# Optimization experiments

Measured on AMD Instinct MI355X. Metric: run time of the kernel, lower is better.

## Reference

```python
import jax, jax.numpy as jnp
import numpy as np

DIM = 768
H = 12          # num_heads
KV = 4          # kv_heads
D = DIM // H    # head_dim = 64
ROPE_BASE = 10000.0
WINDOW = 8
B, N = 4, 1024


def setup_inputs() -> dict:
    key = jax.random.key(0)
    ks = jax.random.split(key, 8)
    s = 0.02  # weight scale for sane magnitudes
    return {
        "x": jax.random.normal(ks[0], (B, N, DIM), jnp.float32),
        "Wq": jax.random.normal(ks[1], (2 * DIM, DIM), jnp.float32) * s,
        "Wk": jax.random.normal(ks[2], (2 * DIM * KV // H, DIM), jnp.float32) * s,
        "Wv1": jax.random.normal(ks[3], (DIM * KV // H, DIM), jnp.float32) * s,
        "Wv2": jax.random.normal(ks[4], (DIM * KV // H, DIM), jnp.float32) * s,
        "lambda_p": jnp.full((H, 1, 1), -2.0, jnp.float32),
        "Wo": jax.random.normal(ks[5], (DIM, DIM), jnp.float32) * s,
        "bo": jax.random.normal(ks[6], (DIM,), jnp.float32) * s,
    }


def _rotate_half(x):
    x1 = x[..., ::2]
    x2 = x[..., 1::2]
    return jnp.stack([-x2, x1], axis=-1).reshape(x.shape)


def _rope_cos_sin(n, dtype):
    side = int(n ** 0.5)
    if side * side == n:
        h = np.arange(side, dtype=np.float32)
        gh, gw = np.meshgrid(h, h, indexing="ij")
        pos_h, pos_w = gh.reshape(-1), gw.reshape(-1)
    else:
        pos_h = np.arange(n, dtype=np.float32)
        pos_w = np.zeros_like(pos_h)
    dim_half = D // 2
    inv_freq = ROPE_BASE ** (-np.arange(dim_half, dtype=np.float32) / dim_half)
    theta = np.concatenate([pos_h[:, None] * inv_freq[None, :],
                            pos_w[:, None] * inv_freq[None, :]], axis=1)  # [N, D]
    cos = jnp.asarray(np.cos(theta), dtype)[None, None]  # [1,1,N,D]
    sin = jnp.asarray(np.sin(theta), dtype)[None, None]
    return cos, sin


def _apply_rope(q, cos, sin):
    return q * cos + _rotate_half(q) * sin


def _qk_norm(t):
    return t / (jnp.linalg.norm(t, axis=-1, keepdims=True) + 1e-6)


def _window_mask(n, dtype):
    side = int(n ** 0.5)
    if side * side == n:
        h = np.arange(side)
        gh, gw = np.meshgrid(h, h, indexing="ij")
        coords = np.stack([gh.reshape(-1), gw.reshape(-1)], axis=1)  # [N,2]
        dist = np.abs(coords[:, None, :] - coords[None, :, :]).max(-1)  # Chebyshev
    else:
        idx = np.arange(n)
        dist = np.abs(idx[None, :] - idx[:, None])
    return jnp.asarray(np.where(dist > WINDOW, -np.inf, 0.0).astype(np.float32), dtype)


def _attend(q, k, v, mask):
    # q,k,v: [B,H,N,D]; mask additive [N,N]
    scale = 1.0 / np.sqrt(D)
    scores = jnp.einsum("bhnd,bhmd->bhnm", q, k) * scale + mask
    return jnp.einsum("bhnm,bhmd->bhnd", jax.nn.softmax(scores, axis=-1), v)


def reference(x, Wq, Wk, Wv1, Wv2, lambda_p, Wo, bo):
    b, n, c = x.shape
    rep = H // KV
    q = (x @ Wq.T).reshape(b, n, 2, H, D).transpose(2, 0, 3, 1, 4)   # [2,B,H,N,D]
    k = (x @ Wk.T).reshape(b, n, 2, KV, D).transpose(2, 0, 3, 1, 4)  # [2,B,KV,N,D]
    v1 = (x @ Wv1.T).reshape(b, n, KV, D).transpose(0, 2, 1, 3)      # [B,KV,N,D]
    v2 = (x @ Wv2.T).reshape(b, n, KV, D).transpose(0, 2, 1, 3)
    q1, q2 = q[0], q[1]
    k1, k2 = k[0], k[1]
    # GQA: repeat_interleave over head axis
    k1 = jnp.repeat(k1, rep, axis=1)
    k2 = jnp.repeat(k2, rep, axis=1)
    v1 = jnp.repeat(v1, rep, axis=1)
    v2 = jnp.repeat(v2, rep, axis=1)
    cos, sin = _rope_cos_sin(n, x.dtype)
    q1, q2 = _apply_rope(q1, cos, sin), _apply_rope(q2, cos, sin)
    k1, k2 = _apply_rope(k1, cos, sin), _apply_rope(k2, cos, sin)
    q1, q2, k1, k2 = _qk_norm(q1), _qk_norm(q2), _qk_norm(k1), _qk_norm(k2)
    mask = _window_mask(n, x.dtype)
    out1 = _attend(q1, k1, v1, mask)
    out2 = _attend(q2, k2, v2, mask)
    lam = jax.nn.softplus(lambda_p)  # [H,1,1] broadcasts over [B,H,N,D]
    out = out1 - lam[None] * out2
    out = out.transpose(0, 2, 1, 3).reshape(b, n, c)
    return out @ Wo.T + bo
```

## Files before the change

kernel.cpp:

```cpp
#include <hip/hip_runtime.h>
#include <hip/hip_bf16.h>

#define BATCH 4
#define NSEQ  1024
#define DIM   768
#define NH    12
#define NKV   4
#define HD    64
#define NTOK  (BATCH*NSEQ)

using bf16 = __hip_bfloat16;
typedef __attribute__((ext_vector_type(8))) short short8;
typedef __attribute__((ext_vector_type(4))) float floatx4;
typedef __attribute__((ext_vector_type(4))) unsigned uint4v;

__device__ __forceinline__ float b2f(short x) {
  unsigned u = ((unsigned)(unsigned short)x) << 16;
  return __builtin_bit_cast(float, u);
}
__device__ __forceinline__ unsigned short f2b(float f) {
  unsigned u = __builtin_bit_cast(unsigned, f);
  unsigned r = u + 0x7FFF + ((u >> 16) & 1);
  return (unsigned short)(r >> 16);
}
__device__ __forceinline__ unsigned cvtpk(float lo, float hi) {
  unsigned r;
  asm("v_cvt_pk_bf16_f32 %0, %1, %2" : "=v"(r) : "v"(lo), "v"(hi));
  return r;
}

__device__ __forceinline__ void load_lds_16(const bf16* g, bf16* l) {
  __builtin_amdgcn_global_load_lds(
      (const __attribute__((address_space(1))) void*)g,
      (__attribute__((address_space(3))) void*)l, 16, 0, 0);
}

__global__ __launch_bounds__(256) void cvt_all(
    const float* __restrict__ x,  const float* __restrict__ wq,
    const float* __restrict__ wk, const float* __restrict__ wv1,
    const float* __restrict__ wv2, const float* __restrict__ wo,
    bf16* __restrict__ xb,  bf16* __restrict__ wqb, bf16* __restrict__ wkb,
    bf16* __restrict__ wv1b, bf16* __restrict__ wv2b, bf16* __restrict__ wob)
{
  int i = blockIdx.x * 256 + threadIdx.x;
  const float* s; bf16* d; int off;
  if      (i <  786432) { s = x;   d = xb;   off = i; }
  else if (i < 1081344) { s = wq;  d = wqb;  off = i -  786432; }
  else if (i < 1179648) { s = wk;  d = wkb;  off = i - 1081344; }
  else if (i < 1228800) { s = wv1; d = wv1b; off = i - 1179648; }
  else if (i < 1277952) { s = wv2; d = wv2b; off = i - 1228800; }
  else                  { s = wo;  d = wob;  off = i - 1277952; }
  float4 f = reinterpret_cast<const float4*>(s)[off];
  ushort4 u;
  u.x = f2b(f.x); u.y = f2b(f.y); u.z = f2b(f.z); u.w = f2b(f.w);
  reinterpret_cast<ushort4*>(d)[off] = u;
}

__global__ __launch_bounds__(256, 3) void gemm_qkv(
    const bf16* __restrict__ xb,
    const bf16* __restrict__ Wqb, const bf16* __restrict__ Wkb,
    const bf16* __restrict__ Wv1b, const bf16* __restrict__ Wv2b,
    bf16* __restrict__ Qpk, bf16* __restrict__ Kpk,
    bf16* __restrict__ Vpk1, bf16* __restrict__ Vpk2)
{
  __shared__ __align__(16) bf16 As[128 * 64];
  __shared__ __align__(16) bf16 Ws[128 * 64];

  const int bn = blockIdx.x, bm = blockIdx.y;
  const bf16* Wp;
  if (bn < 12)      Wp = Wqb  + (size_t)bn * 128 * 768;
  else if (bn < 16) Wp = Wkb  + (size_t)(bn - 12) * 128 * 768;
  else if (bn < 18) Wp = Wv1b + (size_t)(bn - 16) * 128 * 768;
  else              Wp = Wv2b + (size_t)(bn - 18) * 128 * 768;

  const int t = threadIdx.x, wave = t >> 6, lane = t & 63;
  const int wm = wave >> 1, wn = wave & 1;
  const int quad = lane >> 4, lr = lane & 15;

  const int srow = wave * 32 + (lane >> 3);
  const int scol = ((lane & 7) ^ (lane >> 3)) * 8;
  const bf16* Ag = xb + (size_t)(bm * 128 + srow) * 768 + scol;
  const bf16* Wg = Wp + (size_t)srow * 768 + scol;
  bf16* Al = As + wave * 32 * 64;
  bf16* Wl = Ws + wave * 32 * 64;

  floatx4 acc[4][4] = {};

  for (int k0 = 0; k0 < 768; k0 += 64) {
    #pragma unroll
    for (int c = 0; c < 4; ++c) {
      load_lds_16(Ag + (size_t)c * 8 * 768 + k0, Al + c * 8 * 64);
      load_lds_16(Wg + (size_t)c * 8 * 768 + k0, Wl + c * 8 * 64);
    }
    __syncthreads();

    short8 af[4][2], wf[4][2];
    #pragma unroll
    for (int mt = 0; mt < 4; ++mt)
      #pragma unroll
      for (int ks = 0; ks < 2; ++ks)
        af[mt][ks] = *reinterpret_cast<const short8*>(
            &As[(wm * 64 + mt * 16 + lr) * 64 + ((ks * 32 + quad * 8) ^ ((lr & 7) * 8))]);
    #pragma unroll
    for (int nt = 0; nt < 4; ++nt)
      #pragma unroll
      for (int ks = 0; ks < 2; ++ks)
        wf[nt][ks] = *reinterpret_cast<const short8*>(
            &Ws[(wn * 64 + nt * 16 + lr) * 64 + ((ks * 32 + quad * 8) ^ ((lr & 7) * 8))]);

    #pragma unroll
    for (int mt = 0; mt < 4; ++mt)
      #pragma unroll
      for (int nt = 0; nt < 4; ++nt) {
        acc[mt][nt] = __builtin_amdgcn_mfma_f32_16x16x32_bf16(af[mt][0], wf[nt][0], acc[mt][nt], 0, 0, 0);
        acc[mt][nt] = __builtin_amdgcn_mfma_f32_16x16x32_bf16(af[mt][1], wf[nt][1], acc[mt][nt], 0, 0, 0);
      }
    __syncthreads();
  }

  if (bn < 16) {
    const float K2 = 0.41524101186098309f;
    const float invf0 = exp2f(-(float)lr * K2);
    const float invf1 = exp2f(-(float)(16 + lr) * K2);
    const float sgn = (lr & 1) ? 1.f : -1.f;
    const bool isq = (bn < 12);
    const int hq = bn * 2 + wn;
    const int sq_ = hq / 12, hq_ = hq % 12;
    const int hh = (bn - 12) * 2 + wn;
    const int sk_ = hh >> 2, kvh_ = hh & 3;
    const int qk128 = (lr >> 3) * 128;
    #pragma unroll
    for (int mt = 0; mt < 4; ++mt) {
      const int row0 = bm * 128 + wm * 64 + mt * 16 + quad * 4;
      const int n0 = row0 & (NSEQ - 1);
      const int bb = row0 >> 10, kh = n0 >> 5;
      const float ph = (float)kh;
      const float pw0 = (float)(n0 & 31);
      const float t0 = ph * invf0, t1 = ph * invf1;
      const float c0 = __cosf(t0), s0 = __sinf(t0);
      const float c1 = __cosf(t1), s1 = __sinf(t1);
      bf16* tb0;
      if (isq) {
        tb0 = Qpk + ((size_t)((bb * 2 + sq_) * 12 + hq_) * 32 + kh) * 2048
              + (size_t)(mt & 1) * 1024 + qk128 + (quad * 4) * 8 + (lr & 7);
      } else {
        tb0 = Kpk + ((size_t)((bb * 2 + sk_) * 4 + kvh_) * 32 + kh) * 2048
              + (size_t)(mt & 1) * 1024 + qk128 + (quad * 4) * 8 + (lr & 7);
      }
      #pragma unroll
      for (int r = 0; r < 4; ++r) {
        float v0 = acc[mt][0][r];
        float v1 = acc[mt][1][r];
        float v2 = acc[mt][2][r];
        float v3 = acc[mt][3][r];
        float rot0 = sgn * __shfl_xor(v0, 1);
        float rot1 = sgn * __shfl_xor(v1, 1);
        float rot2 = sgn * __shfl_xor(v2, 1);
        float rot3 = sgn * __shfl_xor(v3, 1);
        float pw = pw0 + (float)r;
        float t2 = pw * invf0, t3 = pw * invf1;
        float rv0 = v0 * c0 + rot0 * s0;
        float rv1 = v1 * c1 + rot1 * s1;
        float rv2 = v2 * __cosf(t2) + rot2 * __sinf(t2);
        float rv3 = v3 * __cosf(t3) + rot3 * __sinf(t3);
        float ss = rv0 * rv0 + rv1 * rv1 + rv2 * rv2 + rv3 * rv3;
        #pragma unroll
        for (int off = 1; off < 16; off <<= 1) ss += __shfl_xor(ss, off);
        float sc = 1.f / (sqrtf(ss) + 1e-6f);
        if (isq) sc *= 0.18033688011112042f;
        bf16* tb = tb0 + r * 8;
        unsigned pkA = cvtpk(rv0 * sc, rv1 * sc);
        unsigned pkB = cvtpk(rv2 * sc, rv3 * sc);
        *(unsigned short*)&tb[0]   = (unsigned short)pkA;
        *(unsigned short*)&tb[256] = (unsigned short)(pkA >> 16);
        *(unsigned short*)&tb[512] = (unsigned short)pkB;
        *(unsigned short*)&tb[768] = (unsigned short)(pkB >> 16);
      }
    }
  } else {
    const bool is2 = (bn >= 18);
    bf16* Vp = is2 ? Vpk2 : Vpk1;
    const int kvh_ = (bn - (is2 ? 18 : 16)) * 2 + wn;
    #pragma unroll
    for (int mt = 0; mt < 4; ++mt)
      #pragma unroll
      for (int r = 0; r < 4; ++r) {
        int row = bm * 128 + wm * 64 + mt * 16 + quad * 4 + r;
        int n = row & (NSEQ - 1);
        int bb = row >> 10, kh = n >> 5;
        int rowm = (mt & 1) * 16 + quad * 4 + r;
        int quad_v = (rowm >> 2) & 3;
        int j = ((rowm >> 4) << 2) | (rowm & 3);
        bf16* tb = Vp + ((size_t)(bb * 4 + kvh_) * 32 + kh) * 2048
                   + quad_v * 128 + lr * 8 + j;
        unsigned pkA = cvtpk(acc[mt][0][r], acc[mt][1][r]);
        unsigned pkB = cvtpk(acc[mt][2][r], acc[mt][3][r]);
        *(unsigned short*)&tb[0]    = (unsigned short)pkA;
        *(unsigned short*)&tb[512]  = (unsigned short)(pkA >> 16);
        *(unsigned short*)&tb[1024] = (unsigned short)pkB;
        *(unsigned short*)&tb[1536] = (unsigned short)(pkB >> 16);
      }
  }
}

__global__ __launch_bounds__(256) void gemm_out(
    const bf16* __restrict__ Xb, const bf16* __restrict__ Wob,
    float* __restrict__ out, const float* __restrict__ bias)
{
  __shared__ __align__(16) bf16 As[64 * 64];
  __shared__ __align__(16) bf16 Ws[64 * 64];

  const int bn = blockIdx.x, bm = blockIdx.y;
  const int t = threadIdx.x, wave = t >> 6, lane = t & 63;
  const int wm = wave >> 1, wn = wave & 1;
  const int quad = lane >> 4, lr = lane & 15;

  const int srow = wave * 16 + (lane >> 3);
  const int scol = ((lane & 7) ^ (lane >> 3)) * 8;
  const bf16* Ag = Xb  + (size_t)(bm * 64 + srow) * 768 + scol;
  const bf16* Wg = Wob + (size_t)(bn * 64 + srow) * 768 + scol;
  bf16* Al = As + wave * 16 * 64;
  bf16* Wl = Ws + wave * 16 * 64;

  floatx4 acc[2][2] = {};

  for (int k0 = 0; k0 < 768; k0 += 64) {
    #pragma unroll
    for (int c = 0; c < 2; ++c) {
      load_lds_16(Ag + (size_t)c * 8 * 768 + k0, Al + c * 8 * 64);
      load_lds_16(Wg + (size_t)c * 8 * 768 + k0, Wl + c * 8 * 64);
    }
    __syncthreads();

    short8 af[2][2], wf[2][2];
    #pragma unroll
    for (int mt = 0; mt < 2; ++mt)
      #pragma unroll
      for (int ks = 0; ks < 2; ++ks)
        af[mt][ks] = *reinterpret_cast<const short8*>(
            &As[(wm * 32 + mt * 16 + lr) * 64 + ((ks * 32 + quad * 8) ^ ((lr & 7) * 8))]);
    #pragma unroll
    for (int nt = 0; nt < 2; ++nt)
      #pragma unroll
      for (int ks = 0; ks < 2; ++ks)
        wf[nt][ks] = *reinterpret_cast<const short8*>(
            &Ws[(wn * 32 + nt * 16 + lr) * 64 + ((ks * 32 + quad * 8) ^ ((lr & 7) * 8))]);

    #pragma unroll
    for (int mt = 0; mt < 2; ++mt)
      #pragma unroll
      for (int nt = 0; nt < 2; ++nt) {
        acc[mt][nt] = __builtin_amdgcn_mfma_f32_16x16x32_bf16(af[mt][0], wf[nt][0], acc[mt][nt], 0, 0, 0);
        acc[mt][nt] = __builtin_amdgcn_mfma_f32_16x16x32_bf16(af[mt][1], wf[nt][1], acc[mt][nt], 0, 0, 0);
      }
    __syncthreads();
  }

  #pragma unroll
  for (int nt = 0; nt < 2; ++nt) {
    int col = bn * 64 + wn * 32 + nt * 16 + lr;
    float bv = bias[col];
    #pragma unroll
    for (int mt = 0; mt < 2; ++mt)
      #pragma unroll
      for (int r = 0; r < 4; ++r) {
        int row = bm * 64 + wm * 32 + mt * 16 + quad * 4 + r;
        out[(size_t)row * 768 + col] = acc[mt][nt][r] + bv;
      }
  }
}

struct Frag { short8 kf[2][2]; short8 vf[4]; };

__device__ __forceinline__ void attn_load(
    Frag& f, const bf16* __restrict__ kp, const bf16* __restrict__ vp,
    int kh, int lane8)
{
  const bf16* kt = kp + (size_t)kh * 2048 + lane8;
  const bf16* vt = vp + (size_t)kh * 2048 + lane8;
  f.kf[0][0] = *reinterpret_cast<const short8*>(kt);
  f.kf[0][1] = *reinterpret_cast<const short8*>(kt + 512);
  f.kf[1][0] = *reinterpret_cast<const short8*>(kt + 1024);
  f.kf[1][1] = *reinterpret_cast<const short8*>(kt + 1536);
  f.vf[0] = *reinterpret_cast<const short8*>(vt);
  f.vf[1] = *reinterpret_cast<const short8*>(vt + 512);
  f.vf[2] = *reinterpret_cast<const short8*>(vt + 1024);
  f.vf[3] = *reinterpret_cast<const short8*>(vt + 1536);
}

__device__ __forceinline__ void attn_step(
    const short8 (&qf)[2][2], const Frag& f, const floatx4 (&Sinit)[2][2],
    floatx4 (&O)[2][4], float (&psum)[2])
{
  floatx4 St[2][2] = {{Sinit[0][0], Sinit[0][1]}, {Sinit[1][0], Sinit[1][1]}};
  __builtin_amdgcn_s_setprio(1);
  #pragma unroll
  for (int ks = 0; ks < 2; ++ks) {
    St[0][0] = __builtin_amdgcn_mfma_f32_16x16x32_bf16(f.kf[0][ks], qf[0][ks], St[0][0], 0, 0, 0);
    St[0][1] = __builtin_amdgcn_mfma_f32_16x16x32_bf16(f.kf[0][ks], qf[1][ks], St[0][1], 0, 0, 0);
    St[1][0] = __builtin_amdgcn_mfma_f32_16x16x32_bf16(f.kf[1][ks], qf[0][ks], St[1][0], 0, 0, 0);
    St[1][1] = __builtin_amdgcn_mfma_f32_16x16x32_bf16(f.kf[1][ks], qf[1][ks], St[1][1], 0, 0, 0);
  }
  __builtin_amdgcn_s_setprio(0);

  unsigned pk[2][2][2];
  #pragma unroll
  for (int kt = 0; kt < 2; ++kt)
    #pragma unroll
    for (int mt = 0; mt < 2; ++mt) {
      float pr[4];
      #pragma unroll
      for (int r = 0; r < 4; ++r) {
        float p = __builtin_amdgcn_exp2f(St[kt][mt][r]);
        psum[mt] += p;
        pr[r] = p;
      }
      pk[kt][mt][0] = cvtpk(pr[0], pr[1]);
      pk[kt][mt][1] = cvtpk(pr[2], pr[3]);
    }

  __builtin_amdgcn_s_setprio(1);
  #pragma unroll
  for (int mt = 0; mt < 2; ++mt) {
    uint4v regs;
    regs[0] = pk[0][mt][0];
    regs[1] = pk[0][mt][1];
    regs[2] = pk[1][mt][0];
    regs[3] = pk[1][mt][1];
    short8 pa = __builtin_bit_cast(short8, regs);
    #pragma unroll
    for (int ntd = 0; ntd < 4; ++ntd)
      O[mt][ntd] = __builtin_amdgcn_mfma_f32_16x16x32_bf16(pa, f.vf[ntd], O[mt][ntd], 0, 0, 0);
  }
  __builtin_amdgcn_s_setprio(0);
}

__global__ __launch_bounds__(256, 3) void attn_mfma(
    const bf16* __restrict__ Qpk, const bf16* __restrict__ Kpk,
    const bf16* __restrict__ Vpk1, const bf16* __restrict__ Vpk2,
    const float* __restrict__ lambda_p, bf16* __restrict__ X)
{
  __shared__ __align__(16) char smem[20480];

  const int bid = blockIdx.x;
  const int qh = bid & 31;
  const int hb = bid >> 5;
  const int h  = hb % 12;
  const int b  = hb / 12;
  const int kvh = h / 3;

  const int t = threadIdx.x;
  const int w = t >> 6;
  const int s = w >> 1;
  const int half = w & 1;
  const int lane = t & 63;
  const int quad = lane >> 4, lr = lane & 15;
  const int lane8 = lane * 8;

  float* myO = (float*)(smem + (s ? 10240 : 0));
  float* myP = (float*)(smem + (s ? 10240 : 0) + 8192);
  bf16* Xs = (bf16*)smem;

  const int tok0 = b * NSEQ + qh * 32;

  short8 qf[2][2];
  {
    const bf16* qt = Qpk + ((size_t)((b * 2 + s) * 12 + h) * 32 + qh) * 2048 + lane8;
    qf[0][0] = *reinterpret_cast<const short8*>(qt);
    qf[0][1] = *reinterpret_cast<const short8*>(qt + 512);
    qf[1][0] = *reinterpret_cast<const short8*>(qt + 1024);
    qf[1][1] = *reinterpret_cast<const short8*>(qt + 1536);
  }

  floatx4 Sinit[2][2];
  #pragma unroll
  for (int kt = 0; kt < 2; ++kt)
    #pragma unroll
    for (int mt = 0; mt < 2; ++mt)
      #pragma unroll
      for (int r = 0; r < 4; ++r) {
        int wk = kt * 16 + quad * 4 + r;
        int wq = mt * 16 + lr;
        int d = wk - wq; if (d < 0) d = -d;
        Sinit[kt][mt][r] = (d <= 8) ? 0.0f : -1e38f;
      }

  floatx4 O[2][4] = {};
  float psum[2] = {};

  const int kh0 = (qh > 8) ? qh - 8 : 0;
  const int kh1 = (qh < 23) ? qh + 8 : 31;
  const int cnt = kh1 - kh0 + 1;
  const int cA = (cnt + 1) >> 1;
  const int khA = half ? kh0 + cA : kh0;
  const int khB = half ? kh1 : kh0 + cA - 1;

  const bf16* kpbase = Kpk + (size_t)((b * 2 + s) * 4 + kvh) * 32 * 2048;
  const bf16* vpbase = (s ? Vpk2 : Vpk1) + (size_t)(b * 4 + kvh) * 32 * 2048;

  Frag fA, fB;
  attn_load(fA, kpbase, vpbase, khA, lane8);
  attn_load(fB, kpbase, vpbase, (khA + 1 <= khB) ? khA + 1 : khB, lane8);

  int i = khA;
  while (true) {
    attn_step(qf, fA, Sinit, O, psum);
    if (i == khB) break;
    ++i;
    attn_load(fA, kpbase, vpbase, (i + 1 <= khB) ? i + 1 : i, lane8);
    attn_step(qf, fB, Sinit, O, psum);
    if (i == khB) break;
    ++i;
    attn_load(fB, kpbase, vpbase, (i + 1 <= khB) ? i + 1 : i, lane8);
  }

  auto writeslab = [&]() {
    #pragma unroll
    for (int mt = 0; mt < 2; ++mt)
      #pragma unroll
      for (int ntd = 0; ntd < 4; ++ntd)
        *reinterpret_cast<floatx4*>(&myO[(mt * 4 + ntd) * 256 + lane * 4]) = O[mt][ntd];
    myP[lane]      = psum[0];
    myP[64 + lane] = psum[1];
  };
  auto readadd_norm = [&]() {
    #pragma unroll
    for (int mt = 0; mt < 2; ++mt)
      #pragma unroll
      for (int ntd = 0; ntd < 4; ++ntd)
        O[mt][ntd] += *reinterpret_cast<const floatx4*>(&myO[(mt * 4 + ntd) * 256 + lane * 4]);
    psum[0] += myP[lane];
    psum[1] += myP[64 + lane];
    #pragma unroll
    for (int mt = 0; mt < 2; ++mt) {
      psum[mt] += __shfl_xor(psum[mt], 16);
      psum[mt] += __shfl_xor(psum[mt], 32);
      psum[mt] = 1.f / psum[mt];
    }
    #pragma unroll
    for (int mt = 0; mt < 2; ++mt) {
      float invq[4];
      #pragma unroll
      for (int r = 0; r < 4; ++r)
        invq[r] = __shfl(psum[mt], (lane & 48) + quad * 4 + r);
      #pragma unroll
      for (int ntd = 0; ntd < 4; ++ntd)
        #pragma unroll
        for (int r = 0; r < 4; ++r)
          O[mt][ntd][r] *= invq[r];
    }
  };

  __syncthreads();
  if (half) writeslab();
  __syncthreads();
  if (!half) {
    readadd_norm();
    if (s) {
      #pragma unroll
      for (int mt = 0; mt < 2; ++mt)
        #pragma unroll
        for (int ntd = 0; ntd < 4; ++ntd)
          *reinterpret_cast<floatx4*>(&myO[(mt * 4 + ntd) * 256 + lane * 4]) = O[mt][ntd];
    }
  }
  __syncthreads();
  if (w == 0) {
    const float* O2s = (const float*)(smem + 10240);
    float lam = log1pf(__expf(lambda_p[h]));
    #pragma unroll
    for (int mt = 0; mt < 2; ++mt)
      #pragma unroll
      for (int ntd = 0; ntd < 4; ++ntd) {
        floatx4 o2 = *reinterpret_cast<const floatx4*>(&O2s[(mt * 4 + ntd) * 256 + lane * 4]);
        #pragma unroll
        for (int r = 0; r < 4; ++r) {
          float xv = O[mt][ntd][r] - lam * o2[r];
          *(unsigned short*)&Xs[(mt * 16 + quad * 4 + r) * 72 + ntd * 16 + lr] = f2b(xv);
        }
      }
  }
  __syncthreads();

  {
    int row = t >> 3, seg = t & 7;
    short8 xv = *reinterpret_cast<const short8*>(&Xs[row * 72 + seg * 8]);
    *reinterpret_cast<short8*>(X + (size_t)(tok0 + row) * 768 + h * 64 + seg * 8) = xv;
  }
}

extern "C" void kernel_launch(void* const* d_in, const int* in_sizes, int n_in,
                              void* d_out, int out_size, void* d_ws, size_t ws_size,
                              hipStream_t stream)
{
  const float* x        = (const float*)d_in[0];
  const float* Wq       = (const float*)d_in[1];
  const float* Wk       = (const float*)d_in[2];
  const float* Wv1      = (const float*)d_in[3];
  const float* Wv2      = (const float*)d_in[4];
  const float* lambda_p = (const float*)d_in[5];
  const float* Wo       = (const float*)d_in[6];
  const float* bo       = (const float*)d_in[7];
  float* out = (float*)d_out;

  bf16* xb   = (bf16*)d_ws;
  bf16* Wqb  = xb   + (size_t)NTOK * 768;
  bf16* Wkb  = Wqb  + (size_t)1536 * 768;
  bf16* Wv1b = Wkb  + (size_t)512 * 768;
  bf16* Wv2b = Wv1b + (size_t)256 * 768;
  bf16* Wob  = Wv2b + (size_t)256 * 768;
  bf16* Qpk  = Wob  + (size_t)768 * 768;
  bf16* Xb   = Qpk  + (size_t)NTOK * 1536;
  bf16* Vpk1 = Xb   + (size_t)NTOK * 768;
  bf16* Vpk2 = Vpk1 + (size_t)512 * 2048;
  bf16* Kpk  = Vpk2 + (size_t)512 * 2048;

  cvt_all<<<5568, 256, 0, stream>>>(x, Wq, Wk, Wv1, Wv2, Wo,
                                    xb, Wqb, Wkb, Wv1b, Wv2b, Wob);

  gemm_qkv<<<dim3(20, 32), 256, 0, stream>>>(xb, Wqb, Wkb, Wv1b, Wv2b,
                                             Qpk, Kpk, Vpk1, Vpk2);

  attn_mfma<<<BATCH * NH * 32, 256, 0, stream>>>(Qpk, Kpk, Vpk1, Vpk2, lambda_p, Xb);

  gemm_out<<<dim3(12, 64), 256, 0, stream>>>(Xb, Wob, out, bo);
}
```

Measured before the change: 140.8 us.

## Switch windowed attention to 32x32x16 MFMA tiles with repacked Q/K/V layouts

Replaces the 16x16x32 bf16 MFMA tiling in the attention inner loop with 32x32x16 MFMAs, so each wave computes the 32x32 score block with 4 instructions instead of 8 and the PV product with 4 larger ones instead of 8. The QKV projection epilogue is changed to write the packed Q/K/V fragments in the layout the new MFMA operands expect. The softmax row-sum reduction, normalization and output write-back are remapped to the 32x32 accumulator layout. This reduces instruction issue and shuffle overhead, at the cost of larger accumulators (more registers) and longer-latency MFMAs.

```diff
diff --git a/kernel.cpp b/kernel.cpp
--- a/kernel.cpp
+++ b/kernel.cpp
@@ -12,6 +12,7 @@
 using bf16 = __hip_bfloat16;
 typedef __attribute__((ext_vector_type(8))) short short8;
 typedef __attribute__((ext_vector_type(4))) float floatx4;
+typedef __attribute__((ext_vector_type(16))) float floatx16;
 typedef __attribute__((ext_vector_type(4))) unsigned uint4v;
 
 __device__ __forceinline__ float b2f(short x) {
@@ -128,7 +129,7 @@
     const int sq_ = hq / 12, hq_ = hq % 12;
     const int hh = (bn - 12) * 2 + wn;
     const int sk_ = hh >> 2, kvh_ = hh & 3;
-    const int qk128 = (lr >> 3) * 128;
+    const int fo_lr = (lr >> 3) * 256 + (lr & 7);
     #pragma unroll
     for (int mt = 0; mt < 4; ++mt) {
       const int row0 = bm * 128 + wm * 64 + mt * 16 + quad * 4;
@@ -142,10 +143,10 @@
       bf16* tb0;
       if (isq) {
         tb0 = Qpk + ((size_t)((bb * 2 + sq_) * 12 + hq_) * 32 + kh) * 2048
-              + (size_t)(mt & 1) * 1024 + qk128 + (quad * 4) * 8 + (lr & 7);
+              + fo_lr + ((mt & 1) * 16 + quad * 4) * 8;
       } else {
         tb0 = Kpk + ((size_t)((bb * 2 + sk_) * 4 + kvh_) * 32 + kh) * 2048
-              + (size_t)(mt & 1) * 1024 + qk128 + (quad * 4) * 8 + (lr & 7);
+              + fo_lr + ((mt & 1) * 16 + quad * 4) * 8;
       }
       #pragma unroll
       for (int r = 0; r < 4; ++r) {
@@ -171,10 +172,10 @@
         bf16* tb = tb0 + r * 8;
         unsigned pkA = cvtpk(rv0 * sc, rv1 * sc);
         unsigned pkB = cvtpk(rv2 * sc, rv3 * sc);
-        *(unsigned short*)&tb[0]   = (unsigned short)pkA;
-        *(unsigned short*)&tb[256] = (unsigned short)(pkA >> 16);
-        *(unsigned short*)&tb[512] = (unsigned short)pkB;
-        *(unsigned short*)&tb[768] = (unsigned short)(pkB >> 16);
+        *(unsigned short*)&tb[0]    = (unsigned short)pkA;
+        *(unsigned short*)&tb[512]  = (unsigned short)(pkA >> 16);
+        *(unsigned short*)&tb[1024] = (unsigned short)pkB;
+        *(unsigned short*)&tb[1536] = (unsigned short)(pkB >> 16);
       }
     }
   } else {
@@ -189,16 +190,17 @@
         int n = row & (NSEQ - 1);
         int bb = row >> 10, kh = n >> 5;
         int rowm = (mt & 1) * 16 + quad * 4 + r;
-        int quad_v = (rowm >> 2) & 3;
-        int j = ((rowm >> 4) << 2) | (rowm & 3);
+        int s_ = rowm >> 4;
+        int g_ = (rowm >> 2) & 1;
+        int j  = ((rowm >> 3) & 1) * 4 + (rowm & 3);
         bf16* tb = Vp + ((size_t)(bb * 4 + kvh_) * 32 + kh) * 2048
-                   + quad_v * 128 + lr * 8 + j;
+                   + s_ * 512 + (g_ * 32 + lr) * 8 + j;
         unsigned pkA = cvtpk(acc[mt][0][r], acc[mt][1][r]);
         unsigned pkB = cvtpk(acc[mt][2][r], acc[mt][3][r]);
         *(unsigned short*)&tb[0]    = (unsigned short)pkA;
-        *(unsigned short*)&tb[512]  = (unsigned short)(pkA >> 16);
+        *(unsigned short*)&tb[128]  = (unsigned short)(pkA >> 16);
         *(unsigned short*)&tb[1024] = (unsigned short)pkB;
-        *(unsigned short*)&tb[1536] = (unsigned short)(pkB >> 16);
+        *(unsigned short*)&tb[1152] = (unsigned short)(pkB >> 16);
       }
   }
 }
@@ -270,7 +272,7 @@
   }
 }
 
-struct Frag { short8 kf[2][2]; short8 vf[4]; };
+struct Frag { short8 kf[4]; short8 vf[4]; };
 
 __device__ __forceinline__ void attn_load(
     Frag& f, const bf16* __restrict__ kp, const bf16* __restrict__ vp,
@@ -278,10 +280,10 @@
 {
   const bf16* kt = kp + (size_t)kh * 2048 + lane8;
   const bf16* vt = vp + (size_t)kh * 2048 + lane8;
-  f.kf[0][0] = *reinterpret_cast<const short8*>(kt);
-  f.kf[0][1] = *reinterpret_cast<const short8*>(kt + 512);
-  f.kf[1][0] = *reinterpret_cast<const short8*>(kt + 1024);
-  f.kf[1][1] = *reinterpret_cast<const short8*>(kt + 1536);
+  f.kf[0] = *reinterpret_cast<const short8*>(kt);
+  f.kf[1] = *reinterpret_cast<const short8*>(kt + 512);
+  f.kf[2] = *reinterpret_cast<const short8*>(kt + 1024);
+  f.kf[3] = *reinterpret_cast<const short8*>(kt + 1536);
   f.vf[0] = *reinterpret_cast<const short8*>(vt);
   f.vf[1] = *reinterpret_cast<const short8*>(vt + 512);
   f.vf[2] = *reinterpret_cast<const short8*>(vt + 1024);
@@ -289,49 +291,37 @@
 }
 
 __device__ __forceinline__ void attn_step(
-    const short8 (&qf)[2][2], const Frag& f, const floatx4 (&Sinit)[2][2],
-    floatx4 (&O)[2][4], float (&psum)[2])
-{
-  floatx4 St[2][2] = {{Sinit[0][0], Sinit[0][1]}, {Sinit[1][0], Sinit[1][1]}};
+    const short8 (&qf)[4], const Frag& f, const floatx16& Sinit,
+    floatx16 (&O)[2], float& psum)
+{
+  floatx16 St = Sinit;
   __builtin_amdgcn_s_setprio(1);
   #pragma unroll
-  for (int ks = 0; ks < 2; ++ks) {
-    St[0][0] = __builtin_amdgcn_mfma_f32_16x16x32_bf16(f.kf[0][ks], qf[0][ks], St[0][0], 0, 0, 0);
-    St[0][1] = __builtin_amdgcn_mfma_f32_16x16x32_bf16(f.kf[0][ks], qf[1][ks], St[0][1], 0, 0, 0);
-    St[1][0] = __builtin_amdgcn_mfma_f32_16x16x32_bf16(f.kf[1][ks], qf[0][ks], St[1][0], 0, 0, 0);
-    St[1][1] = __builtin_amdgcn_mfma_f32_16x16x32_bf16(f.kf[1][ks], qf[1][ks], St[1][1], 0, 0, 0);
-  }
+  for (int s = 0; s < 4; ++s)
+    St = __builtin_amdgcn_mfma_f32_32x32x16_bf16(f.kf[s], qf[s], St, 0, 0, 0);
   __builtin_amdgcn_s_setprio(0);
 
-  unsigned pk[2][2][2];
+  float p[16];
   #pragma unroll
-  for (int kt = 0; kt < 2; ++kt)
-    #pragma unroll
-    for (int mt = 0; mt < 2; ++mt) {
-      float pr[4];
-      #pragma unroll
-      for (int r = 0; r < 4; ++r) {
-        float p = __builtin_amdgcn_exp2f(St[kt][mt][r]);
-        psum[mt] += p;
-        pr[r] = p;
-      }
-      pk[kt][mt][0] = cvtpk(pr[0], pr[1]);
-      pk[kt][mt][1] = cvtpk(pr[2], pr[3]);
-    }
+  for (int r = 0; r < 16; ++r) {
+    p[r] = __builtin_amdgcn_exp2f(St[r]);
+    psum += p[r];
+  }
+  unsigned pk[8];
+  #pragma unroll
+  for (int i = 0; i < 8; ++i) pk[i] = cvtpk(p[2 * i], p[2 * i + 1]);
+
+  uint4v r0, r1;
+  r0[0] = pk[0]; r0[1] = pk[1]; r0[2] = pk[2]; r0[3] = pk[3];
+  r1[0] = pk[4]; r1[1] = pk[5]; r1[2] = pk[6]; r1[3] = pk[7];
+  short8 pa0 = __builtin_bit_cast(short8, r0);
+  short8 pa1 = __builtin_bit_cast(short8, r1);
 
   __builtin_amdgcn_s_setprio(1);
-  #pragma unroll
-  for (int mt = 0; mt < 2; ++mt) {
-    uint4v regs;
-    regs[0] = pk[0][mt][0];
-    regs[1] = pk[0][mt][1];
-    regs[2] = pk[1][mt][0];
-    regs[3] = pk[1][mt][1];
-    short8 pa = __builtin_bit_cast(short8, regs);
-    #pragma unroll
-    for (int ntd = 0; ntd < 4; ++ntd)
-      O[mt][ntd] = __builtin_amdgcn_mfma_f32_16x16x32_bf16(pa, f.vf[ntd], O[mt][ntd], 0, 0, 0);
-  }
+  O[0] = __builtin_amdgcn_mfma_f32_32x32x16_bf16(pa0, f.vf[0], O[0], 0, 0, 0);
+  O[0] = __builtin_amdgcn_mfma_f32_32x32x16_bf16(pa1, f.vf[1], O[0], 0, 0, 0);
+  O[1] = __builtin_amdgcn_mfma_f32_32x32x16_bf16(pa0, f.vf[2], O[1], 0, 0, 0);
+  O[1] = __builtin_amdgcn_mfma_f32_32x32x16_bf16(pa1, f.vf[3], O[1], 0, 0, 0);
   __builtin_amdgcn_s_setprio(0);
 }
 
@@ -354,7 +344,7 @@
   const int s = w >> 1;
   const int half = w & 1;
   const int lane = t & 63;
-  const int quad = lane >> 4, lr = lane & 15;
+  const int g = lane >> 5, wq = lane & 31;
   const int lane8 = lane * 8;
 
   float* myO = (float*)(smem + (s ? 10240 : 0));
@@ -363,30 +353,25 @@
 
   const int tok0 = b * NSEQ + qh * 32;
 
-  short8 qf[2][2];
+  short8 qf[4];
   {
     const bf16* qt = Qpk + ((size_t)((b * 2 + s) * 12 + h) * 32 + qh) * 2048 + lane8;
-    qf[0][0] = *reinterpret_cast<const short8*>(qt);
-    qf[0][1] = *reinterpret_cast<const short8*>(qt + 512);
-    qf[1][0] = *reinterpret_cast<const short8*>(qt + 1024);
-    qf[1][1] = *reinterpret_cast<const short8*>(qt + 1536);
-  }
-
-  floatx4 Sinit[2][2];
+    qf[0] = *reinterpret_cast<const short8*>(qt);
+    qf[1] = *reinterpret_cast<const short8*>(qt + 512);
+    qf[2] = *reinterpret_cast<const short8*>(qt + 1024);
+    qf[3] = *reinterpret_cast<const short8*>(qt + 1536);
+  }
+
+  floatx16 Sinit;
   #pragma unroll
-  for (int kt = 0; kt < 2; ++kt)
-    #pragma unroll
-    for (int mt = 0; mt < 2; ++mt)
-      #pragma unroll
-      for (int r = 0; r < 4; ++r) {
-        int wk = kt * 16 + quad * 4 + r;
-        int wq = mt * 16 + lr;
-        int d = wk - wq; if (d < 0) d = -d;
-        Sinit[kt][mt][r] = (d <= 8) ? 0.0f : -1e38f;
-      }
-
-  floatx4 O[2][4] = {};
-  float psum[2] = {};
+  for (int reg = 0; reg < 16; ++reg) {
+    int wk = (reg & 3) + 8 * (reg >> 2) + 4 * g;
+    int d = wk - wq; if (d < 0) d = -d;
+    Sinit[reg] = (d <= 8) ? 0.0f : -1e38f;
+  }
+
+  floatx16 O[2] = {};
+  float psum = 0.f;
 
   const int kh0 = (qh > 8) ? qh - 8 : 0;
   const int kh1 = (qh < 23) ? qh + 8 : 31;
@@ -416,39 +401,37 @@
 
   auto writeslab = [&]() {
     #pragma unroll
-    for (int mt = 0; mt < 2; ++mt)
-      #pragma unroll
-      for (int ntd = 0; ntd < 4; ++ntd)
-        *reinterpret_cast<floatx4*>(&myO[(mt * 4 + ntd) * 256 + lane * 4]) = O[mt][ntd];
-    myP[lane]      = psum[0];
-    myP[64 + lane] = psum[1];
+    for (int pv = 0; pv < 2; ++pv)
+      #pragma unroll
+      for (int rq = 0; rq < 4; ++rq) {
+        floatx4 c;
+        c[0] = O[pv][rq * 4 + 0]; c[1] = O[pv][rq * 4 + 1];
+        c[2] = O[pv][rq * 4 + 2]; c[3] = O[pv][rq * 4 + 3];
+        *reinterpret_cast<floatx4*>(&myO[(pv * 4 + rq) * 256 + lane * 4]) = c;
+      }
+    myP[lane] = psum;
   };
   auto readadd_norm = [&]() {
     #pragma unroll
-    for (int mt = 0; mt < 2; ++mt)
-      #pragma unroll
-      for (int ntd = 0; ntd < 4; ++ntd)
-        O[mt][ntd] += *reinterpret_cast<const floatx4*>(&myO[(mt * 4 + ntd) * 256 + lane * 4]);
-    psum[0] += myP[lane];
-    psum[1] += myP[64 + lane];
-    #pragma unroll
-    for (int mt = 0; mt < 2; ++mt) {
-      psum[mt] += __shfl_xor(psum[mt], 16);
-      psum[mt] += __shfl_xor(psum[mt], 32);
-      psum[mt] = 1.f / psum[mt];
-    }
-    #pragma unroll
-    for (int mt = 0; mt < 2; ++mt) {
-      float invq[4];
-      #pragma unroll
-      for (int r = 0; r < 4; ++r)
-        invq[r] = __shfl(psum[mt], (lane & 48) + quad * 4 + r);
-      #pragma unroll
-      for (int ntd = 0; ntd < 4; ++ntd)
-        #pragma unroll
-        for (int r = 0; r < 4; ++r)
-          O[mt][ntd][r] *= invq[r];
-    }
+    for (int pv = 0; pv < 2; ++pv)
+      #pragma unroll
+      for (int rq = 0; rq < 4; ++rq) {
+        floatx4 c = *reinterpret_cast<const floatx4*>(&myO[(pv * 4 + rq) * 256 + lane * 4]);
+        O[pv][rq * 4 + 0] += c[0]; O[pv][rq * 4 + 1] += c[1];
+        O[pv][rq * 4 + 2] += c[2]; O[pv][rq * 4 + 3] += c[3];
+      }
+    psum += myP[lane];
+    psum += __shfl_xor(psum, 32);
+    float inv = 1.f / psum;
+    float invq[16];
+    #pragma unroll
+    for (int reg = 0; reg < 16; ++reg)
+      invq[reg] = __shfl(inv, (reg & 3) + 8 * (reg >> 2) + 4 * g);
+    #pragma unroll
+    for (int pv = 0; pv < 2; ++pv)
+      #pragma unroll
+      for (int reg = 0; reg < 16; ++reg)
+        O[pv][reg] *= invq[reg];
   };
 
   __syncthreads();
@@ -458,10 +441,14 @@
     readadd_norm();
     if (s) {
       #pragma unroll
-      for (int mt = 0; mt < 2; ++mt)
+      for (int pv = 0; pv < 2; ++pv)
         #pragma unroll
-        for (int ntd = 0; ntd < 4; ++ntd)
-          *reinterpret_cast<floatx4*>(&myO[(mt * 4 + ntd) * 256 + lane * 4]) = O[mt][ntd];
+        for (int rq = 0; rq < 4; ++rq) {
+          floatx4 c;
+          c[0] = O[pv][rq * 4 + 0]; c[1] = O[pv][rq * 4 + 1];
+          c[2] = O[pv][rq * 4 + 2]; c[3] = O[pv][rq * 4 + 3];
+          *reinterpret_cast<floatx4*>(&myO[(pv * 4 + rq) * 256 + lane * 4]) = c;
+        }
     }
   }
   __syncthreads();
@@ -469,14 +456,16 @@
     const float* O2s = (const float*)(smem + 10240);
     float lam = log1pf(__expf(lambda_p[h]));
     #pragma unroll
-    for (int mt = 0; mt < 2; ++mt)
-      #pragma unroll
-      for (int ntd = 0; ntd < 4; ++ntd) {
-        floatx4 o2 = *reinterpret_cast<const floatx4*>(&O2s[(mt * 4 + ntd) * 256 + lane * 4]);
+    for (int pv = 0; pv < 2; ++pv)
+      #pragma unroll
+      for (int rq = 0; rq < 4; ++rq) {
+        floatx4 o2 = *reinterpret_cast<const floatx4*>(&O2s[(pv * 4 + rq) * 256 + lane * 4]);
         #pragma unroll
-        for (int r = 0; r < 4; ++r) {
-          float xv = O[mt][ntd][r] - lam * o2[r];
-          *(unsigned short*)&Xs[(mt * 16 + quad * 4 + r) * 72 + ntd * 16 + lr] = f2b(xv);
+        for (int e = 0; e < 4; ++e) {
+          float xv = O[pv][rq * 4 + e] - lam * o2[e];
+          int q = e + 8 * rq + 4 * g;
+          int d = pv * 32 + wq;
+          *(unsigned short*)&Xs[q * 72 + d] = f2b(xv);
         }
       }
   }
```

After: 141.6 us. Within noise of the previous version (+0.5%).
